# Performance work log

Measured on AMD Instinct MI355X. Metric: run time of the kernel, lower is better.

The kernel has to match this reference:

```python
import jax, jax.numpy as jnp
import numpy as np
import math

B, S, H, NH = 2, 2048, 2048, 16
HD = H // NH
LAYER_NUMBER = 5
NORM_FACTOR = math.sqrt(HD) * LAYER_NUMBER  # sqrt(head_dim) * coeff
BETA = 1.0 / LAYER_NUMBER
SCALE = float(LAYER_NUMBER)  # ScaledSoftmax scale = coeff
MASK_VALUE = -10000.0


def setup_inputs() -> dict:
    key = jax.random.key(0)
    ks = jax.random.split(key, 6)
    inv_sqrt_h = 1.0 / math.sqrt(H)
    return {
        "hidden_states": jax.random.normal(ks[0], (B, S, H), jnp.float32),
        "alibi": jax.random.normal(ks[1], (NH, 1, S), jnp.float32) * 0.1,
        "w_qkv": jax.random.normal(ks[2], (3 * H, H), jnp.float32) * inv_sqrt_h,
        "b_qkv": jax.random.normal(ks[3], (3 * H,), jnp.float32) * 0.02,
        "w_dense": jax.random.normal(ks[4], (H, H), jnp.float32) * inv_sqrt_h,
        "b_dense": jax.random.normal(ks[5], (H,), jnp.float32) * 0.02,
        "attention_mask": jnp.ones((B, S), jnp.int32),
    }


def reference(hidden_states, alibi, w_qkv, b_qkv, w_dense, b_dense, attention_mask):
    b, s, h = hidden_states.shape
    # QKV projection: [b, s, 3h] -> [b, s, nh, 3*hd] -> split
    mixed = hidden_states @ w_qkv.T + b_qkv
    mixed = mixed.reshape(b, s, NH, 3 * HD)
    q, k, v = jnp.split(mixed, 3, axis=-1)  # each [b, s, nh, hd]

    # Faithful Megatron-style memory reinterpretation (row-major reshape),
    # exactly matching torch's .contiguous().view(s, b*nh, hd).
    q2 = jnp.swapaxes(q.reshape(s, b * NH, HD), 0, 1)  # [b*nh, q_len, hd]
    k2 = jnp.swapaxes(k.reshape(s, b * NH, HD), 0, 1)  # [b*nh, k_len, hd]
    v2 = jnp.swapaxes(v.reshape(s, b * NH, HD), 0, 1)  # [b*nh, k_len, hd]

    # baddbmm: alibi*beta + (q @ k^T)/norm_factor
    alibi_b = jnp.tile(alibi, (b, 1, 1))[: b * NH, :, :s]  # [b*nh, 1, k_len]
    scores = alibi_b * BETA + jnp.einsum("bqd,bkd->bqk", q2, k2) * (1.0 / NORM_FACTOR)
    scores = scores.reshape(b, NH, s, s)

    # ScaledSoftmax: scale then fused causal+padding mask fill, then softmax
    scores = scores * SCALE
    pad_bool = (1 - attention_mask).astype(bool)  # True where padded
    causal = jnp.tril(jnp.ones((s, s), dtype=bool))
    bad = pad_bool[:, None, :, None] | (~causal)[None, None, :, :]  # [b,1,s,s]
    scores = jnp.where(bad, MASK_VALUE, scores)
    probs = jax.nn.softmax(scores, axis=-1)  # [b, nh, s, s]

    # context = probs @ V with the same faithful reshapes
    probs_r = probs.reshape(b * NH, s, s)
    context = jnp.einsum("bqk,bkd->bqd", probs_r, v2)  # [b*nh, q_len, hd]
    context = context.reshape(b, NH, s, HD)
    context = jnp.transpose(context, (2, 0, 1, 3)).reshape(s, b, h)  # [s, b, h]

    out = context @ w_dense.T + b_dense  # [s, b, h]
    return jnp.swapaxes(out, 0, 1)  # [b, s, h]
```

## Files before the change

kernel.cpp:

```cpp
#include <hip/hip_runtime.h>

typedef unsigned short u16;
typedef __bf16  bf16x8 __attribute__((ext_vector_type(8)));
typedef float   f32x4  __attribute__((ext_vector_type(4)));
typedef u16     u16x8  __attribute__((ext_vector_type(8)));
typedef u16     u16x4  __attribute__((ext_vector_type(4)));

#define QSCALE 0.12751744545f

__device__ __forceinline__ u16 f2b(float f) {
    unsigned u = __float_as_uint(f);
    unsigned r = u + 0x7FFFu + ((u >> 16) & 1u);
    return (u16)(r >> 16);
}
__device__ __forceinline__ float b2f(u16 b) {
    return __uint_as_float(((unsigned)b) << 16);
}
__device__ __forceinline__ void async16(const u16* g, u16* l) {
    __builtin_amdgcn_global_load_lds(
        (__attribute__((address_space(1))) void*)(u16*)g,
        (__attribute__((address_space(3))) void*)l, 16, 0, 0);
}

__global__ void cvt_f32_bf16(const float* __restrict__ in, u16* __restrict__ out, int n4) {
    int i = blockIdx.x * blockDim.x + threadIdx.x;
    if (i >= n4) return;
    float4 f = ((const float4*)in)[i];
    u16x4 o;
    o[0] = f2b(f.x); o[1] = f2b(f.y); o[2] = f2b(f.z); o[3] = f2b(f.w);
    *(u16x4*)(out + (size_t)i * 4) = o;
}

__global__ void cvt_wqkv(const float* __restrict__ in, u16* __restrict__ out, int n4) {
    int i = blockIdx.x * blockDim.x + threadIdx.x;
    if (i >= n4) return;
    int row = i >> 9;
    float s = ((row % 384) < 128) ? QSCALE : 1.0f;
    float4 f = ((const float4*)in)[i];
    u16x4 o;
    o[0] = f2b(f.x * s); o[1] = f2b(f.y * s); o[2] = f2b(f.z * s); o[3] = f2b(f.w * s);
    *(u16x4*)(out + (size_t)i * 4) = o;
}

__global__ __launch_bounds__(256) void gemm_bt(
    const u16* __restrict__ A, const u16* __restrict__ B,
    const float* __restrict__ bias, void* __restrict__ C,
    u16* __restrict__ qb, u16* __restrict__ kb, u16* __restrict__ vb,
    int M, int N, int K, int mode)
{
    __shared__ u16 smem[16384];
    u16* As = smem;
    u16* Bs = smem + 8192;

    int tid = threadIdx.x, wave = tid >> 6, lane = tid & 63;
    int lg = lane >> 4, lm = lane & 15;
    int wm = (wave & 1) * 64, wn = (wave >> 1) * 64;

    const u16* Ab = A + (size_t)(blockIdx.y * 128) * K;
    const u16* Bb = B + (size_t)(blockIdx.x * 128) * K;

    f32x4 acc[4][4];
    for (int i = 0; i < 4; i++)
        for (int j = 0; j < 4; j++)
            acc[i][j] = (f32x4){0.f, 0.f, 0.f, 0.f};

    int srow = (lane >> 2), skq = (lane & 3) * 8;

    for (int k0 = 0; k0 < K; k0 += 64) {
        __syncthreads();
        for (int cc = wave; cc < 16; cc += 4) {
            int p = cc >> 3, c = cc & 7;
            int row = c * 16 + srow;
            size_t off = (size_t)row * K + k0 + p * 32 + skq;
            async16(Ab + off, &As[p * 4096 + c * 512]);
            async16(Bb + off, &Bs[p * 4096 + c * 512]);
        }
        __syncthreads();

        for (int p = 0; p < 2; p++) {
            bf16x8 af[4], bf[4];
            for (int i = 0; i < 4; i++) af[i] = *(const bf16x8*)&As[p * 4096 + (wm + i * 16 + lm) * 32 + lg * 8];
            for (int j = 0; j < 4; j++) bf[j] = *(const bf16x8*)&Bs[p * 4096 + (wn + j * 16 + lm) * 32 + lg * 8];
            for (int i = 0; i < 4; i++)
                for (int j = 0; j < 4; j++)
                    acc[i][j] = __builtin_amdgcn_mfma_f32_16x16x32_bf16(af[i], bf[j], acc[i][j], 0, 0, 0);
        }
    }

    if (mode == 1) {
        for (int j = 0; j < 4; j++) {
            int col = blockIdx.x * 128 + wn + j * 16 + lm;
            float bv = bias[col];
            for (int i = 0; i < 4; i++) {
                int row0 = blockIdx.y * 128 + wm + i * 16 + lg * 4;
                for (int r = 0; r < 4; r++) {
                    int row = row0 + r;
                    int orow = ((row & 1) << 11) + (row >> 1);
                    ((float*)C)[(size_t)orow * N + col] = acc[i][j][r] + bv;
                }
            }
        }
        return;
    }

    int ct = blockIdx.x;
    int nh = ct / 3, part = ct - nh * 3;
    float bscale = (part == 0) ? QSCALE : 1.0f;
    int rbase = blockIdx.y * 128;
    int b = rbase >> 11;
    int s0 = rbase & 2047;

    if (part < 2) {
        u16* dst0 = part ? kb : qb;
        for (int j = 0; j < 4; j++) {
            int hd = wn + j * 16 + lm;
            float bv = bias[ct * 128 + hd] * bscale;
            for (int i = 0; i < 4; i++) {
                for (int r = 0; r < 4; r++) {
                    int rl = wm + i * 16 + lg * 4 + r;
                    int s = s0 + rl;
                    int bn = (s & 1) * 16 + nh;
                    int pos = (b << 10) + (s >> 1);
                    dst0[((size_t)(bn * 2048 + pos)) * 128 + hd] = f2b(acc[i][j][r] + bv);
                }
            }
        }
    } else {
        u16 (*arr)[64][128] = (u16(*)[64][128])smem;
        __syncthreads();
        for (int j = 0; j < 4; j++) {
            int hd = wn + j * 16 + lm;
            float bv = bias[ct * 128 + hd];
            for (int i = 0; i < 4; i++) {
                for (int r = 0; r < 4; r++) {
                    int rl = wm + i * 16 + lg * 4 + r;
                    arr[rl & 1][rl >> 1][hd] = f2b(acc[i][j][r] + bv);
                }
            }
        }
        __syncthreads();
        int hd = tid & 127, par = tid >> 7;
        int bn = par * 16 + nh;
        int pos0 = (b << 10) + (s0 >> 1);
        u16* dst = vb + ((size_t)(bn * 128 + hd)) * 2048 + pos0;
        for (int c = 0; c < 8; c++) {
            u16x8 w;
            for (int e = 0; e < 8; e++) w[e] = arr[par][c * 8 + e][hd];
            *(u16x8*)(dst + c * 8) = w;
        }
    }
}

__global__ __launch_bounds__(256, 2) void attn(
    const u16* __restrict__ qb, const u16* __restrict__ kb,
    const u16* __restrict__ vb, const float* __restrict__ alibi,
    float* __restrict__ Opart, float* __restrict__ Spart)
{
    __shared__ u16 Ks[64 * 140];
    __shared__ u16 Vt[128 * 90];
    __shared__ u16 Ps[4][32 * 76];

    int j = blockIdx.x, bn = blockIdx.y;
    int tid = threadIdx.x, wave = tid >> 6, lane = tid & 63;
    int lg = lane >> 4, lm = lane & 15;

    const float* al = alibi + (bn & 15) * 2048;

    int krow = tid >> 2, kq = (tid & 3) * 32;
    int vhd  = tid >> 1, vh2 = (tid & 1) * 32;
    const u16* ksrc0 = kb + (size_t)(bn * 2048 + krow) * 128 + kq;
    const u16* vsrc0 = vb + (size_t)(bn * 128 + vhd) * 2048 + vh2;

    u16* ps = &Ps[wave][0];
    bf16x8 ones;
    {
        u16x8 t;
        for (int e = 0; e < 8; e++) t[e] = 0x3F80;
        ones = *(bf16x8*)&t;
    }

    int part, qts[2], kA[2], kB[2];
    if (j < 8) {
        part = 0;
        qts[0] = 15 - j; kA[0] = 0;      kB[0] = 15 - j;
        qts[1] = j;      kA[1] = 0;      kB[1] = j;
    } else {
        part = 1;
        qts[0] = j;      kA[0] = j + 1;  kB[0] = 2 * j + 1;
        qts[1] = 15 - j; kA[1] = 16 - j; kB[1] = 31 - 2 * j;
    }

    for (int s = 0; s < 2; s++) {
        int qt = qts[s], ktA = kA[s], ktB = kB[s];
        int q0w = qt * 128 + wave * 32;

        bf16x8 qf[2][4];
        for (int i = 0; i < 2; i++) {
            const u16* qp = qb + ((size_t)bn * 2048 + q0w + i * 16 + lm) * 128 + lg * 8;
            for (int kc = 0; kc < 4; kc++) qf[i][kc] = *(const bf16x8*)(qp + kc * 32);
        }

        f32x4 o[2][8], sums[2];
        for (int i = 0; i < 2; i++) {
            sums[i] = (f32x4){0.f, 0.f, 0.f, 0.f};
            for (int h = 0; h < 8; h++) o[i][h] = (f32x4){0.f, 0.f, 0.f, 0.f};
        }

        u16x8 kreg[4], vreg[4];
        {
            const u16* s1 = ksrc0 + (size_t)ktA * 64 * 128;
            const u16* s2 = vsrc0 + ktA * 64;
            for (int i = 0; i < 4; i++) kreg[i] = *(const u16x8*)(s1 + i * 8);
            for (int i = 0; i < 4; i++) vreg[i] = *(const u16x8*)(s2 + i * 8);
        }

        for (int kt = ktA; kt <= ktB; kt++) {
            int k0 = kt * 64;
            __syncthreads();
            {
                u16* d1 = &Ks[krow * 140 + kq];
                for (int i = 0; i < 4; i++) *(u16x8*)(d1 + i * 8) = kreg[i];
                u16* d2 = &Vt[vhd * 90 + vh2];
                for (int i = 0; i < 4; i++) *(u16x8*)(d2 + i * 8) = vreg[i];
            }
            __syncthreads();

            if (kt < ktB) {
                const u16* s1 = ksrc0 + (size_t)(kt + 1) * 64 * 128;
                const u16* s2 = vsrc0 + (kt + 1) * 64;
                for (int i = 0; i < 4; i++) kreg[i] = *(const u16x8*)(s1 + i * 8);
                for (int i = 0; i < 4; i++) vreg[i] = *(const u16x8*)(s2 + i * 8);
            }

            bool domask = (k0 + 63 > q0w);
            for (int tc = 0; tc < 4; tc++) {
                const u16* kr = &Ks[(tc * 16 + lm) * 140 + lg * 8];
                f32x4 a0 = (f32x4){0.f, 0.f, 0.f, 0.f};
                f32x4 a1 = (f32x4){0.f, 0.f, 0.f, 0.f};
                for (int kc = 0; kc < 4; kc++) {
                    bf16x8 bfr = *(const bf16x8*)(kr + kc * 32);
                    a0 = __builtin_amdgcn_mfma_f32_16x16x32_bf16(qf[0][kc], bfr, a0, 0, 0, 0);
                    a1 = __builtin_amdgcn_mfma_f32_16x16x32_bf16(qf[1][kc], bfr, a1, 0, 0, 0);
                }
                int kg = k0 + tc * 16 + lm;
                float av = (al[kg] - 8.0f) * 1.4426950408889634f;
                for (int r = 0; r < 4; r++) {
                    float v0 = a0[r] + av, v1 = a1[r] + av;
                    if (domask) {
                        int r0 = q0w + lg * 4 + r;
                        if (kg > r0) v0 = -3e38f;
                        if (kg > r0 + 16) v1 = -3e38f;
                    }
                    ps[(lg * 4 + r) * 76 + tc * 16 + lm]        = f2b(__builtin_amdgcn_exp2f(v0));
                    ps[(16 + lg * 4 + r) * 76 + tc * 16 + lm]   = f2b(__builtin_amdgcn_exp2f(v1));
                }
            }

            for (int kc = 0; kc < 2; kc++) {
                bf16x8 pf0 = *(const bf16x8*)&ps[lm * 76 + kc * 32 + lg * 8];
                bf16x8 pf1 = *(const bf16x8*)&ps[(16 + lm) * 76 + kc * 32 + lg * 8];
                for (int ht = 0; ht < 8; ht++) {
                    bf16x8 vf = *(const bf16x8*)&Vt[(ht * 16 + lm) * 90 + kc * 32 + lg * 8];
                    o[0][ht] = __builtin_amdgcn_mfma_f32_16x16x32_bf16(pf0, vf, o[0][ht], 0, 0, 0);
                    o[1][ht] = __builtin_amdgcn_mfma_f32_16x16x32_bf16(pf1, vf, o[1][ht], 0, 0, 0);
                }
                sums[0] = __builtin_amdgcn_mfma_f32_16x16x32_bf16(pf0, ones, sums[0], 0, 0, 0);
                sums[1] = __builtin_amdgcn_mfma_f32_16x16x32_bf16(pf1, ones, sums[1], 0, 0, 0);
            }
        }

        float* Op = Opart + (((size_t)part * 32 + bn) * 2048 + qt * 128) * 128;
        for (int i = 0; i < 2; i++)
            for (int r = 0; r < 4; r++) {
                int row = wave * 32 + i * 16 + lg * 4 + r;
                float* orow = Op + (size_t)row * 128 + lm;
                for (int ht = 0; ht < 8; ht++) orow[ht * 16] = o[i][ht][r];
            }
        if (lm == 0) {
            float* Sp = Spart + ((size_t)part * 32 + bn) * 2048 + qt * 128 + wave * 32;
            for (int i = 0; i < 2; i++)
                for (int r = 0; r < 4; r++)
                    Sp[i * 16 + lg * 4 + r] = sums[i][r];
        }
    }
}

__global__ void attn_fin(const float* __restrict__ Opart, const float* __restrict__ Spart,
                         u16* __restrict__ ctx)
{
    int idx = blockIdx.x * 256 + threadIdx.x;
    int hd8 = idx & 15;
    int q   = (idx >> 4) & 2047;
    int bn  = idx >> 15;
    size_t o0 = (((size_t)bn) * 2048 + q) * 128 + hd8 * 8;
    size_t o1 = (size_t)32 * 2048 * 128 + o0;
    float s = Spart[bn * 2048 + q] + Spart[32 * 2048 + bn * 2048 + q];
    float inv = 1.0f / s;
    const float4* A = (const float4*)(Opart + o0);
    const float4* B = (const float4*)(Opart + o1);
    float4 a0 = A[0], a1 = A[1], b0 = B[0], b1 = B[1];
    u16x8 w;
    w[0] = f2b((a0.x + b0.x) * inv); w[1] = f2b((a0.y + b0.y) * inv);
    w[2] = f2b((a0.z + b0.z) * inv); w[3] = f2b((a0.w + b0.w) * inv);
    w[4] = f2b((a1.x + b1.x) * inv); w[5] = f2b((a1.y + b1.y) * inv);
    w[6] = f2b((a1.z + b1.z) * inv); w[7] = f2b((a1.w + b1.w) * inv);
    *(u16x8*)(ctx + ((size_t)(q * 2 + (bn >> 4))) * 2048 + (bn & 15) * 128 + hd8 * 8) = w;
}

extern "C" void kernel_launch(void* const* d_in, const int* in_sizes, int n_in,
                              void* d_out, int out_size, void* d_ws, size_t ws_size,
                              hipStream_t stream)
{
    const float* hs    = (const float*)d_in[0];
    const float* alibi = (const float*)d_in[1];
    const float* wqkv  = (const float*)d_in[2];
    const float* bqkv  = (const float*)d_in[3];
    const float* wd    = (const float*)d_in[4];
    const float* bd    = (const float*)d_in[5];
    float* out = (float*)d_out;

    char* ws = (char*)d_ws;
    u16*   wqkv_b = (u16*)(ws + 0);
    u16*   hs_b   = (u16*)(ws + 25165824);
    float* Opart  = (float*)(ws + 0);
    u16*   ctx    = (u16*)(ws + 67108864);
    u16*   wd_b   = (u16*)(ws + 83886080);
    u16*   qb     = (u16*)(ws + 92274688);
    u16*   kb     = (u16*)(ws + 109051904);
    u16*   vb     = (u16*)(ws + 125829120);
    float* Spart  = (float*)d_out;

    cvt_f32_bf16<<<8192,  256, 0, stream>>>(hs,   hs_b,   2097152);
    cvt_wqkv   <<<12288, 256, 0, stream>>>(wqkv, wqkv_b, 3145728);

    gemm_bt<<<dim3(48, 32), 256, 0, stream>>>(hs_b, wqkv_b, bqkv, nullptr,
                                              qb, kb, vb, 4096, 6144, 2048, 0);

    cvt_f32_bf16<<<4096, 256, 0, stream>>>(wd, wd_b, 1048576);

    attn<<<dim3(16, 32), 256, 0, stream>>>(qb, kb, vb, alibi, Opart, Spart);
    attn_fin<<<4096, 256, 0, stream>>>(Opart, Spart, ctx);

    gemm_bt<<<dim3(16, 32), 256, 0, stream>>>(ctx, wd_b, bd, out,
                                              nullptr, nullptr, nullptr, 4096, 2048, 2048, 1);
}
```

Measured before the change: 463.8 us.

## Load K/V tiles with async global-to-LDS copies and store partial outputs in bf16

The attention kernel now copies K and V tiles straight into LDS with global_load_lds instead of staging them through registers, and rearranges the LDS layout into unpadded 32-column chunks per wave. The register prefetch of the next tile is removed, so loads are no longer overlapped with compute. The partial output buffers are written as bf16 instead of fp32, which halves the traffic between the attention and finalize kernels at some cost in precision. The unpadded LDS layout may also cause bank conflicts on reads.

```diff
diff --git a/kernel.cpp b/kernel.cpp
--- a/kernel.cpp
+++ b/kernel.cpp
@@ -154,10 +154,10 @@
 __global__ __launch_bounds__(256, 2) void attn(
     const u16* __restrict__ qb, const u16* __restrict__ kb,
     const u16* __restrict__ vb, const float* __restrict__ alibi,
-    float* __restrict__ Opart, float* __restrict__ Spart)
+    u16* __restrict__ Opart, float* __restrict__ Spart)
 {
-    __shared__ u16 Ks[64 * 140];
-    __shared__ u16 Vt[128 * 90];
+    __shared__ u16 Ks[4 * 2048];
+    __shared__ u16 Vt[2 * 4096];
     __shared__ u16 Ps[4][32 * 76];
 
     int j = blockIdx.x, bn = blockIdx.y;
@@ -166,10 +166,11 @@
 
     const float* al = alibi + (bn & 15) * 2048;
 
-    int krow = tid >> 2, kq = (tid & 3) * 32;
-    int vhd  = tid >> 1, vh2 = (tid & 1) * 32;
-    const u16* ksrc0 = kb + (size_t)(bn * 2048 + krow) * 128 + kq;
-    const u16* vsrc0 = vb + (size_t)(bn * 128 + vhd) * 2048 + vh2;
+    const u16* kK = kb + ((size_t)bn * 2048 + (lane >> 2)) * 128 + wave * 32 + (lane & 3) * 8;
+    const u16* kV = vb + ((size_t)(bn * 128 + (wave & 1) * 64 + (lane >> 2))) * 2048
+                       + (wave >> 1) * 32 + (lane & 3) * 8;
+    u16* KsW = Ks + wave * 2048;
+    u16* VtW = Vt + (wave >> 1) * 4096 + (wave & 1) * 2048;
 
     u16* ps = &Ps[wave][0];
     bf16x8 ones;
@@ -206,39 +207,25 @@
             for (int h = 0; h < 8; h++) o[i][h] = (f32x4){0.f, 0.f, 0.f, 0.f};
         }
 
-        u16x8 kreg[4], vreg[4];
-        {
-            const u16* s1 = ksrc0 + (size_t)ktA * 64 * 128;
-            const u16* s2 = vsrc0 + ktA * 64;
-            for (int i = 0; i < 4; i++) kreg[i] = *(const u16x8*)(s1 + i * 8);
-            for (int i = 0; i < 4; i++) vreg[i] = *(const u16x8*)(s2 + i * 8);
-        }
-
         for (int kt = ktA; kt <= ktB; kt++) {
             int k0 = kt * 64;
             __syncthreads();
             {
-                u16* d1 = &Ks[krow * 140 + kq];
-                for (int i = 0; i < 4; i++) *(u16x8*)(d1 + i * 8) = kreg[i];
-                u16* d2 = &Vt[vhd * 90 + vh2];
-                for (int i = 0; i < 4; i++) *(u16x8*)(d2 + i * 8) = vreg[i];
+                const u16* kg = kK + (size_t)k0 * 128;
+                const u16* vg = kV + k0;
+                for (int i = 0; i < 4; i++) {
+                    async16(kg + (size_t)i * 2048, KsW + i * 512);
+                    async16(vg + (size_t)i * 32768, VtW + i * 512);
+                }
             }
             __syncthreads();
-
-            if (kt < ktB) {
-                const u16* s1 = ksrc0 + (size_t)(kt + 1) * 64 * 128;
-                const u16* s2 = vsrc0 + (kt + 1) * 64;
-                for (int i = 0; i < 4; i++) kreg[i] = *(const u16x8*)(s1 + i * 8);
-                for (int i = 0; i < 4; i++) vreg[i] = *(const u16x8*)(s2 + i * 8);
-            }
 
             bool domask = (k0 + 63 > q0w);
             for (int tc = 0; tc < 4; tc++) {
-                const u16* kr = &Ks[(tc * 16 + lm) * 140 + lg * 8];
                 f32x4 a0 = (f32x4){0.f, 0.f, 0.f, 0.f};
                 f32x4 a1 = (f32x4){0.f, 0.f, 0.f, 0.f};
                 for (int kc = 0; kc < 4; kc++) {
-                    bf16x8 bfr = *(const bf16x8*)(kr + kc * 32);
+                    bf16x8 bfr = *(const bf16x8*)&Ks[kc * 2048 + (tc * 16 + lm) * 32 + lg * 8];
                     a0 = __builtin_amdgcn_mfma_f32_16x16x32_bf16(qf[0][kc], bfr, a0, 0, 0, 0);
                     a1 = __builtin_amdgcn_mfma_f32_16x16x32_bf16(qf[1][kc], bfr, a1, 0, 0, 0);
                 }
@@ -251,8 +238,8 @@
                         if (kg > r0) v0 = -3e38f;
                         if (kg > r0 + 16) v1 = -3e38f;
                     }
-                    ps[(lg * 4 + r) * 76 + tc * 16 + lm]        = f2b(__builtin_amdgcn_exp2f(v0));
-                    ps[(16 + lg * 4 + r) * 76 + tc * 16 + lm]   = f2b(__builtin_amdgcn_exp2f(v1));
+                    ps[(lg * 4 + r) * 76 + tc * 16 + lm]      = f2b(__builtin_amdgcn_exp2f(v0));
+                    ps[(16 + lg * 4 + r) * 76 + tc * 16 + lm] = f2b(__builtin_amdgcn_exp2f(v1));
                 }
             }
 
@@ -260,7 +247,7 @@
                 bf16x8 pf0 = *(const bf16x8*)&ps[lm * 76 + kc * 32 + lg * 8];
                 bf16x8 pf1 = *(const bf16x8*)&ps[(16 + lm) * 76 + kc * 32 + lg * 8];
                 for (int ht = 0; ht < 8; ht++) {
-                    bf16x8 vf = *(const bf16x8*)&Vt[(ht * 16 + lm) * 90 + kc * 32 + lg * 8];
+                    bf16x8 vf = *(const bf16x8*)&Vt[kc * 4096 + (ht * 16 + lm) * 32 + lg * 8];
                     o[0][ht] = __builtin_amdgcn_mfma_f32_16x16x32_bf16(pf0, vf, o[0][ht], 0, 0, 0);
                     o[1][ht] = __builtin_amdgcn_mfma_f32_16x16x32_bf16(pf1, vf, o[1][ht], 0, 0, 0);
                 }
@@ -269,12 +256,12 @@
             }
         }
 
-        float* Op = Opart + (((size_t)part * 32 + bn) * 2048 + qt * 128) * 128;
+        u16* Op = Opart + (((size_t)part * 32 + bn) * 2048 + qt * 128) * 128;
         for (int i = 0; i < 2; i++)
             for (int r = 0; r < 4; r++) {
                 int row = wave * 32 + i * 16 + lg * 4 + r;
-                float* orow = Op + (size_t)row * 128 + lm;
-                for (int ht = 0; ht < 8; ht++) orow[ht * 16] = o[i][ht][r];
+                u16* orow = Op + (size_t)row * 128 + lm;
+                for (int ht = 0; ht < 8; ht++) orow[ht * 16] = f2b(o[i][ht][r]);
             }
         if (lm == 0) {
             float* Sp = Spart + ((size_t)part * 32 + bn) * 2048 + qt * 128 + wave * 32;
@@ -285,7 +272,7 @@
     }
 }
 
-__global__ void attn_fin(const float* __restrict__ Opart, const float* __restrict__ Spart,
+__global__ void attn_fin(const u16* __restrict__ Opart, const float* __restrict__ Spart,
                          u16* __restrict__ ctx)
 {
     int idx = blockIdx.x * 256 + threadIdx.x;
@@ -293,17 +280,13 @@
     int q   = (idx >> 4) & 2047;
     int bn  = idx >> 15;
     size_t o0 = (((size_t)bn) * 2048 + q) * 128 + hd8 * 8;
-    size_t o1 = (size_t)32 * 2048 * 128 + o0;
+    size_t o1 = o0 + (size_t)32 * 2048 * 128;
     float s = Spart[bn * 2048 + q] + Spart[32 * 2048 + bn * 2048 + q];
     float inv = 1.0f / s;
-    const float4* A = (const float4*)(Opart + o0);
-    const float4* B = (const float4*)(Opart + o1);
-    float4 a0 = A[0], a1 = A[1], b0 = B[0], b1 = B[1];
+    u16x8 a = *(const u16x8*)(Opart + o0);
+    u16x8 b = *(const u16x8*)(Opart + o1);
     u16x8 w;
-    w[0] = f2b((a0.x + b0.x) * inv); w[1] = f2b((a0.y + b0.y) * inv);
-    w[2] = f2b((a0.z + b0.z) * inv); w[3] = f2b((a0.w + b0.w) * inv);
-    w[4] = f2b((a1.x + b1.x) * inv); w[5] = f2b((a1.y + b1.y) * inv);
-    w[6] = f2b((a1.z + b1.z) * inv); w[7] = f2b((a1.w + b1.w) * inv);
+    for (int e = 0; e < 8; e++) w[e] = f2b((b2f(a[e]) + b2f(b[e])) * inv);
     *(u16x8*)(ctx + ((size_t)(q * 2 + (bn >> 4))) * 2048 + (bn & 15) * 128 + hd8 * 8) = w;
 }
 
@@ -322,7 +305,7 @@
     char* ws = (char*)d_ws;
     u16*   wqkv_b = (u16*)(ws + 0);
     u16*   hs_b   = (u16*)(ws + 25165824);
-    float* Opart  = (float*)(ws + 0);
+    u16*   Opart  = (u16*)(ws + 0);
     u16*   ctx    = (u16*)(ws + 67108864);
     u16*   wd_b   = (u16*)(ws + 83886080);
     u16*   qb     = (u16*)(ws + 92274688);
```

Measured after the change: 402.0 us. 1.15x faster.
